# Kernel optimization log

Measured on AMD Instinct MI355X. Metric: run time of the kernel, lower is better.

## Reference

```python
import jax, jax.numpy as jnp
import numpy as np

B = 16384
HIST_LEN, DYN_DIM, STAT_DIM, TIME_DIM = 24, 8, 3, 8
N_STATIONS, EMB_DIM = 120, 16
IN_DIM = HIST_LEN * DYN_DIM + STAT_DIM + TIME_DIM + EMB_DIM  # 219
HIDDEN, OUT = 64, 1
GRID, K = 5, 3
NUM_BASIS = GRID + K  # 8


def make_grid(in_dim):
    # uniform extended grid on [-1, 1], pykan-style: G + 2k + 1 knots per input
    h = 2.0 / GRID
    pts = jnp.arange(-K, GRID + K + 1, dtype=jnp.float32) * h - 1.0  # [G+2k+1]
    return jnp.broadcast_to(pts, (in_dim, pts.shape[0]))


def b_splines(x, grid_pts):
    # x: [B, I], grid_pts: [I, G+2k+1] -> bases [B, I, G+k] via Cox-de Boor
    g = grid_pts[None]              # [1, I, M]
    xe = x[..., None]               # [B, I, 1]
    b = ((xe >= g[..., :-1]) & (xe < g[..., 1:])).astype(x.dtype)
    for p in range(1, K + 1):
        b = ((xe - g[..., : -(p + 1)]) / (g[..., p:-1] - g[..., : -(p + 1)]) * b[..., :-1]
             + (g[..., p + 1:] - xe) / (g[..., p + 1:] - g[..., 1:-p]) * b[..., 1:])
    return b  # [B, I, G+k]


def kan_layer(x, w_base, coef, grid_pts):
    # base path (silu residual) + spline path
    y_base = jax.nn.silu(x) @ w_base                              # [B, O]
    y_spline = jnp.einsum('big,iog->bo', b_splines(x, grid_pts), coef)
    return y_base + y_spline


def setup_inputs() -> dict:
    key = jax.random.key(0)
    ks = jax.random.split(key, 9)
    hist = jax.random.normal(ks[0], (B, HIST_LEN, DYN_DIM), dtype=jnp.float32)
    static = jax.random.normal(ks[1], (B, STAT_DIM), dtype=jnp.float32)
    time_feats = jax.random.normal(ks[2], (B, TIME_DIM), dtype=jnp.float32)
    st_idx = jax.random.randint(ks[3], (B,), 0, N_STATIONS)
    emb_table = jax.random.normal(ks[4], (N_STATIONS, EMB_DIM), dtype=jnp.float32)
    s1 = 1.0 / np.sqrt(IN_DIM)
    s2 = 1.0 / np.sqrt(HIDDEN)
    w_base1 = jax.random.normal(ks[5], (IN_DIM, HIDDEN), dtype=jnp.float32) * s1
    coef1 = jax.random.normal(ks[6], (IN_DIM, HIDDEN, NUM_BASIS), dtype=jnp.float32) * (0.1 * s1)
    w_base2 = jax.random.normal(ks[7], (HIDDEN, OUT), dtype=jnp.float32) * s2
    coef2 = jax.random.normal(ks[8], (HIDDEN, OUT, NUM_BASIS), dtype=jnp.float32) * (0.1 * s2)
    return {"hist": hist, "static": static, "time_feats": time_feats, "st_idx": st_idx,
            "emb_table": emb_table, "w_base1": w_base1, "coef1": coef1,
            "w_base2": w_base2, "coef2": coef2}


def reference(hist, static, time_feats, st_idx, emb_table, w_base1, coef1, w_base2, coef2):
    grid1 = make_grid(IN_DIM)
    grid2 = make_grid(HIDDEN)
    hist_flat = hist.reshape(hist.shape[0], -1)          # [B, hist_len*dyn_dim]
    emb = emb_table[st_idx]                              # [B, emb_dim]
    x = jnp.concatenate([hist_flat, static, time_feats, emb], axis=1)  # [B, 219]
    h = kan_layer(x, w_base1, coef1, grid1)              # [B, 64]
    out = kan_layer(h, w_base2, coef2, grid2)            # [B, 1]
    return out.squeeze(-1)                               # [B]
```

## Files before the change

### kernel.cpp

```cpp
#include <hip/hip_runtime.h>


typedef _Float16 half8 __attribute__((ext_vector_type(8)));
typedef float floatx4 __attribute__((ext_vector_type(4)));

#define NTILES 7
#define QSTEPS 9
#define FROW   296

__device__ __forceinline__ float silu_f(float x) {
    return x / (1.0f + __expf(-x));
}

__device__ __forceinline__ void bspline8(float x, float f[8]) {
    float u  = (x + 2.2f) * 2.5f;
    float fj = floorf(u);
    float t  = u - fj;
    int   j  = (int)fj;
    bool valid = (u >= 0.0f) && (u < 11.0f);
    float t2 = t * t, t3 = t2 * t;
    float omt = 1.0f - t;
    float b0 = omt * omt * omt * (1.0f / 6.0f);
    float b1 = (3.0f * t3 - 6.0f * t2 + 4.0f) * (1.0f / 6.0f);
    float b2 = (-3.0f * t3 + 3.0f * t2 + 3.0f * t + 1.0f) * (1.0f / 6.0f);
    float b3 = t3 * (1.0f / 6.0f);
    if (!valid) { b0 = b1 = b2 = b3 = 0.0f; }
    int base = j - 3;
#pragma unroll
    for (int g = 0; g < 8; ++g) {
        int m = g - base;
        float v = (m == 0) ? b0 : 0.0f;
        v = (m == 1) ? b1 : v;
        v = (m == 2) ? b2 : v;
        v = (m == 3) ? b3 : v;
        f[g] = v;
    }
}

__global__ __launch_bounds__(256) void build_w(
    const float* __restrict__ wb1, const float* __restrict__ cf1,
    _Float16* __restrict__ wcat)
{
    int flat = blockIdx.x * 256 + threadIdx.x;
    int j    = flat & 7;
    int l    = (flat >> 3) & 63;
    int nt   = (flat >> 9) & 3;
    int step = flat >> 11;
    int t    = step / QSTEPS;
    int q    = step - t * QSTEPS;
    int kl   = q * 32 + ((l >> 4) << 3) + j;
    int n    = nt * 16 + (l & 15);
    float v  = 0.0f;
    if (kl < 32) {
        int i = t * 32 + kl;
        if (i < 219) v = wb1[i * 64 + n];
    } else {
        int sp = kl - 32;
        int i  = t * 32 + (sp >> 3);
        int g  = sp & 7;
        if (i < 219) v = cf1[(i * 64 + n) * 8 + g];
    }
    wcat[flat] = (_Float16)v;
}

__global__ __launch_bounds__(256) void kan_mfma(
    const float* __restrict__ hist,
    const float* __restrict__ statf,
    const float* __restrict__ timef,
    const int*   __restrict__ st_idx,
    const float* __restrict__ emb,
    const _Float16* __restrict__ wcat,
    const float* __restrict__ wb2,
    const float* __restrict__ cf2,
    float* __restrict__ out)
{
    __shared__ union {
        _Float16 feat[32 * FROW];
        struct { float h[32 * 65]; float part[8 * 32]; } ep;
    } sm;

    const int tid  = threadIdx.x;
    const int lane = tid & 63;
    const int w    = __builtin_amdgcn_readfirstlane(tid >> 6);
    const int bx   = blockIdx.x;

    const int iloc = tid & 31;
    const int sg   = tid >> 5;

    floatx4 acc[2];
    acc[0] = (floatx4){0.f, 0.f, 0.f, 0.f};
    acc[1] = (floatx4){0.f, 0.f, 0.f, 0.f};

    for (int t = 0; t < NTILES; ++t) {
        const int i = t * 32 + iloc;
        __syncthreads();
#pragma unroll
        for (int r = 0; r < 4; ++r) {
            const int s = sg * 4 + r;
            const int b = bx * 32 + s;
            float sv = 0.0f;
            half8 spl = (half8)(_Float16)0.0f;
            if (i < 219) {
                float x;
                if (i < 192)      x = hist[b * 192 + i];
                else if (i < 195) x = statf[b * 3 + (i - 192)];
                else if (i < 203) x = timef[b * 8 + (i - 195)];
                else              x = emb[st_idx[b] * 16 + (i - 203)];
                sv = silu_f(x);
                float f[8];
                bspline8(x, f);
#pragma unroll
                for (int g = 0; g < 8; ++g) spl[g] = (_Float16)f[g];
            }
            sm.feat[s * FROW + iloc] = (_Float16)sv;
            *(half8*)&sm.feat[s * FROW + 32 + iloc * 8] = spl;
        }
        __syncthreads();
#pragma unroll
        for (int q = 0; q < QSTEPS; ++q) {
            half8 bfrag = *(const half8*)(wcat + (size_t)(((t * QSTEPS + q) * 4 + w) * 64 + lane) * 8);
            const int koff = q * 32 + ((lane >> 4) << 3);
#pragma unroll
            for (int mt = 0; mt < 2; ++mt) {
                half8 afrag = *(const half8*)&sm.feat[(mt * 16 + (lane & 15)) * FROW + koff];
                acc[mt] = __builtin_amdgcn_mfma_f32_16x16x32_f16(afrag, bfrag, acc[mt], 0, 0, 0);
            }
        }
    }

    __syncthreads();
#pragma unroll
    for (int mt = 0; mt < 2; ++mt) {
#pragma unroll
        for (int r = 0; r < 4; ++r) {
            const int row = mt * 16 + ((lane >> 4) << 2) + r;
            const int col = w * 16 + (lane & 15);
            sm.ep.h[row * 65 + col] = acc[mt][r];
        }
    }
    __syncthreads();

    {
        const int s  = tid & 31;
        const int og = tid >> 5;
        float psum = 0.0f;
#pragma unroll
        for (int oo = 0; oo < 8; ++oo) {
            const int o = og * 8 + oo;
            float h = sm.ep.h[s * 65 + o];
            psum = fmaf(silu_f(h), wb2[o], psum);
            float f2[8];
            bspline8(h, f2);
#pragma unroll
            for (int g = 0; g < 8; ++g)
                psum = fmaf(f2[g], cf2[o * 8 + g], psum);
        }
        sm.ep.part[og * 32 + s] = psum;
    }
    __syncthreads();
    if (tid < 32) {
        float r = 0.0f;
#pragma unroll
        for (int og = 0; og < 8; ++og) r += sm.ep.part[og * 32 + tid];
        out[bx * 32 + tid] = r;
    }
}

extern "C" void kernel_launch(void* const* d_in, const int* in_sizes, int n_in,
                              void* d_out, int out_size, void* d_ws, size_t ws_size,
                              hipStream_t stream) {
    const float* hist  = (const float*)d_in[0];
    const float* statf = (const float*)d_in[1];
    const float* timef = (const float*)d_in[2];
    const int*   stidx = (const int*)  d_in[3];
    const float* emb   = (const float*)d_in[4];
    const float* wb1   = (const float*)d_in[5];
    const float* cf1   = (const float*)d_in[6];
    const float* wb2   = (const float*)d_in[7];
    const float* cf2   = (const float*)d_in[8];
    float* out = (float*)d_out;

    _Float16* wcat = (_Float16*)d_ws;

    build_w<<<504, 256, 0, stream>>>(wb1, cf1, wcat);
    kan_mfma<<<512, 256, 0, stream>>>(hist, statf, timef, stidx, emb,
                                      wcat, wb2, cf2, out);
}
```

Before: 110.4 us.

## Stage raw inputs in LDS and build MFMA A-fragments in registers with split-K waves

The kernel now loads raw x values into shared memory once with vectorized float4 loads. Each wave computes its silu and B-spline A-fragments directly in registers: the spline fragment comes from a 64-bit shift of four packed fp16 basis values, replacing the dense 8-way select and the fp16 feature tile in LDS. The weight layout is reordered so that each K-step holds either 32 silu inputs or 4 inputs × 8 bases. Waves split M and K, and the two K halves are summed in the epilogue. This removes the per-tile barriers and the LDS feature writes, but each wave now recomputes the features for its own rows.

```diff
diff --git a/kernel.cpp b/kernel.cpp
--- a/kernel.cpp
+++ b/kernel.cpp
@@ -4,22 +4,19 @@
 typedef _Float16 half8 __attribute__((ext_vector_type(8)));
 typedef float floatx4 __attribute__((ext_vector_type(4)));
 
-#define NTILES 7
-#define QSTEPS 9
-#define FROW   296
+#define XR 233
 
 __device__ __forceinline__ float silu_f(float x) {
     return x / (1.0f + __expf(-x));
 }
 
-__device__ __forceinline__ void bspline8(float x, float f[8]) {
+__device__ __forceinline__ void bspline8_dense(float x, float f[8]) {
     float u  = (x + 2.2f) * 2.5f;
     float fj = floorf(u);
     float t  = u - fj;
     int   j  = (int)fj;
     bool valid = (u >= 0.0f) && (u < 11.0f);
-    float t2 = t * t, t3 = t2 * t;
-    float omt = 1.0f - t;
+    float t2 = t * t, t3 = t2 * t, omt = 1.0f - t;
     float b0 = omt * omt * omt * (1.0f / 6.0f);
     float b1 = (3.0f * t3 - 6.0f * t2 + 4.0f) * (1.0f / 6.0f);
     float b2 = (-3.0f * t3 + 3.0f * t2 + 3.0f * t + 1.0f) * (1.0f / 6.0f);
@@ -37,30 +34,62 @@
     }
 }
 
+__device__ __forceinline__ half8 bspline_frag(float x) {
+    float u  = (x + 2.2f) * 2.5f;
+    float fj = floorf(u);
+    float t  = u - fj;
+    int   j  = (int)fj;
+    bool valid = (u >= 0.0f) && (u < 11.0f);
+    float t2 = t * t, t3 = t2 * t, omt = 1.0f - t;
+    float b0 = omt * omt * omt * (1.0f / 6.0f);
+    float b1 = (3.0f * t3 - 6.0f * t2 + 4.0f) * (1.0f / 6.0f);
+    float b2 = (-3.0f * t3 + 3.0f * t2 + 3.0f * t + 1.0f) * (1.0f / 6.0f);
+    float b3 = t3 * (1.0f / 6.0f);
+    union { _Float16 h[4]; unsigned long long q; } p;
+    p.h[0] = (_Float16)b0; p.h[1] = (_Float16)b1;
+    p.h[2] = (_Float16)b2; p.h[3] = (_Float16)b3;
+    unsigned long long lo = valid ? p.q : 0ull;
+    int jc = valid ? j : 3;
+    int sh = (jc - 3) * 16;
+    unsigned long long rlo, rhi;
+    if (sh >= 0) {
+        rlo = (sh < 64) ? (lo << sh) : 0ull;
+        rhi = (sh == 0) ? 0ull
+            : (sh < 64) ? (lo >> (64 - sh))
+                        : (lo << (sh - 64));
+    } else {
+        rlo = lo >> (-sh);
+        rhi = 0ull;
+    }
+    union { unsigned long long q[2]; half8 v; } r;
+    r.q[0] = rlo; r.q[1] = rhi;
+    return r.v;
+}
+
 __global__ __launch_bounds__(256) void build_w(
     const float* __restrict__ wb1, const float* __restrict__ cf1,
     _Float16* __restrict__ wcat)
 {
     int flat = blockIdx.x * 256 + threadIdx.x;
-    int j    = flat & 7;
-    int l    = (flat >> 3) & 63;
-    int nt   = (flat >> 9) & 3;
-    int step = flat >> 11;
-    int t    = step / QSTEPS;
-    int q    = step - t * QSTEPS;
-    int kl   = q * 32 + ((l >> 4) << 3) + j;
-    int n    = nt * 16 + (l & 15);
-    float v  = 0.0f;
-    if (kl < 32) {
-        int i = t * 32 + kl;
-        if (i < 219) v = wb1[i * 64 + n];
+    int lane = flat & 63;
+    int nt   = (flat >> 6) & 3;
+    int st   = flat >> 8;
+    int kg   = lane >> 4;
+    int n    = nt * 16 + (lane & 15);
+    _Float16 v[8];
+    if (st < 7) {
+#pragma unroll
+        for (int j = 0; j < 8; ++j) {
+            int i = st * 32 + kg * 8 + j;
+            v[j] = (_Float16)((i < 219) ? wb1[i * 64 + n] : 0.0f);
+        }
     } else {
-        int sp = kl - 32;
-        int i  = t * 32 + (sp >> 3);
-        int g  = sp & 7;
-        if (i < 219) v = cf1[(i * 64 + n) * 8 + g];
-    }
-    wcat[flat] = (_Float16)v;
+        int i = (st - 7) * 4 + kg;
+#pragma unroll
+        for (int j = 0; j < 8; ++j)
+            v[j] = (_Float16)((i < 219) ? cf1[(i * 64 + n) * 8 + j] : 0.0f);
+    }
+    *(half8*)(wcat + (size_t)flat * 8) = *(half8*)v;
 }
 
 __global__ __launch_bounds__(256) void kan_mfma(
@@ -75,67 +104,95 @@
     float* __restrict__ out)
 {
     __shared__ union {
-        _Float16 feat[32 * FROW];
-        struct { float h[32 * 65]; float part[8 * 32]; } ep;
+        float xb[32 * XR];
+        struct { float h[2][32 * 65]; float part[8 * 32]; } ep;
     } sm;
 
     const int tid  = threadIdx.x;
     const int lane = tid & 63;
     const int w    = __builtin_amdgcn_readfirstlane(tid >> 6);
+    const int mt   = w & 1;
+    const int kh   = w >> 1;
     const int bx   = blockIdx.x;
-
-    const int iloc = tid & 31;
-    const int sg   = tid >> 5;
-
-    floatx4 acc[2];
-    acc[0] = (floatx4){0.f, 0.f, 0.f, 0.f};
-    acc[1] = (floatx4){0.f, 0.f, 0.f, 0.f};
-
-    for (int t = 0; t < NTILES; ++t) {
-        const int i = t * 32 + iloc;
-        __syncthreads();
+    const int row  = lane & 15;
+    const int kg   = lane >> 4;
+
+    {
+        const int s = tid >> 3, q4 = tid & 7;
+        const int b = bx * 32 + s;
+        const float4* h4 = (const float4*)hist;
+#pragma unroll
+        for (int f = 0; f < 6; ++f) {
+            int i4 = q4 + 8 * f;
+            float4 v = h4[b * 48 + i4];
+            sm.xb[s * XR + i4 * 4 + 0] = v.x;
+            sm.xb[s * XR + i4 * 4 + 1] = v.y;
+            sm.xb[s * XR + i4 * 4 + 2] = v.z;
+            sm.xb[s * XR + i4 * 4 + 3] = v.w;
+        }
+    }
+#pragma unroll
+    for (int f = 0; f < 4; ++f) {
+        int flat = f * 256 + tid;
+        int s  = flat >> 5;
+        int ii = 192 + (flat & 31);
+        int b  = bx * 32 + s;
+        float v;
+        if (ii < 195)      v = statf[b * 3 + (ii - 192)];
+        else if (ii < 203) v = timef[b * 8 + (ii - 195)];
+        else if (ii < 219) v = emb[st_idx[b] * 16 + (ii - 203)];
+        else               v = 0.0f;
+        sm.xb[s * XR + ii] = v;
+    }
+    __syncthreads();
+
+    const float* xrow = &sm.xb[(mt * 16 + row) * XR];
+
+    floatx4 acc[4];
+#pragma unroll
+    for (int nt = 0; nt < 4; ++nt) acc[nt] = (floatx4){0.f, 0.f, 0.f, 0.f};
+
+    for (int st = kh; st < 7; st += 2) {
+        const _Float16* wp = wcat + (size_t)(st * 4) * 512 + lane * 8;
+        half8 bf0 = *(const half8*)(wp);
+        half8 bf1 = *(const half8*)(wp + 512);
+        half8 bf2 = *(const half8*)(wp + 1024);
+        half8 bf3 = *(const half8*)(wp + 1536);
+        const int i0 = st * 32 + kg * 8;
+        half8 af;
+#pragma unroll
+        for (int jj = 0; jj < 8; ++jj)
+            af[jj] = (_Float16)silu_f(xrow[i0 + jj]);
+        acc[0] = __builtin_amdgcn_mfma_f32_16x16x32_f16(af, bf0, acc[0], 0, 0, 0);
+        acc[1] = __builtin_amdgcn_mfma_f32_16x16x32_f16(af, bf1, acc[1], 0, 0, 0);
+        acc[2] = __builtin_amdgcn_mfma_f32_16x16x32_f16(af, bf2, acc[2], 0, 0, 0);
+        acc[3] = __builtin_amdgcn_mfma_f32_16x16x32_f16(af, bf3, acc[3], 0, 0, 0);
+    }
+
+    const int st0 = (kh == 1) ? 7 : 8;
+#pragma unroll 2
+    for (int st = st0; st < 63; st += 2) {
+        const _Float16* wp = wcat + (size_t)(st * 4) * 512 + lane * 8;
+        half8 bf0 = *(const half8*)(wp);
+        half8 bf1 = *(const half8*)(wp + 512);
+        half8 bf2 = *(const half8*)(wp + 1024);
+        half8 bf3 = *(const half8*)(wp + 1536);
+        float x = xrow[(st - 7) * 4 + kg];
+        half8 af = bspline_frag(x);
+        acc[0] = __builtin_amdgcn_mfma_f32_16x16x32_f16(af, bf0, acc[0], 0, 0, 0);
+        acc[1] = __builtin_amdgcn_mfma_f32_16x16x32_f16(af, bf1, acc[1], 0, 0, 0);
+        acc[2] = __builtin_amdgcn_mfma_f32_16x16x32_f16(af, bf2, acc[2], 0, 0, 0);
+        acc[3] = __builtin_amdgcn_mfma_f32_16x16x32_f16(af, bf3, acc[3], 0, 0, 0);
+    }
+
+    __syncthreads();
+#pragma unroll
+    for (int nt = 0; nt < 4; ++nt) {
 #pragma unroll
         for (int r = 0; r < 4; ++r) {
-            const int s = sg * 4 + r;
-            const int b = bx * 32 + s;
-            float sv = 0.0f;
-            half8 spl = (half8)(_Float16)0.0f;
-            if (i < 219) {
-                float x;
-                if (i < 192)      x = hist[b * 192 + i];
-                else if (i < 195) x = statf[b * 3 + (i - 192)];
-                else if (i < 203) x = timef[b * 8 + (i - 195)];
-                else              x = emb[st_idx[b] * 16 + (i - 203)];
-                sv = silu_f(x);
-                float f[8];
-                bspline8(x, f);
-#pragma unroll
-                for (int g = 0; g < 8; ++g) spl[g] = (_Float16)f[g];
-            }
-            sm.feat[s * FROW + iloc] = (_Float16)sv;
-            *(half8*)&sm.feat[s * FROW + 32 + iloc * 8] = spl;
-        }
-        __syncthreads();
-#pragma unroll
-        for (int q = 0; q < QSTEPS; ++q) {
-            half8 bfrag = *(const half8*)(wcat + (size_t)(((t * QSTEPS + q) * 4 + w) * 64 + lane) * 8);
-            const int koff = q * 32 + ((lane >> 4) << 3);
-#pragma unroll
-            for (int mt = 0; mt < 2; ++mt) {
-                half8 afrag = *(const half8*)&sm.feat[(mt * 16 + (lane & 15)) * FROW + koff];
-                acc[mt] = __builtin_amdgcn_mfma_f32_16x16x32_f16(afrag, bfrag, acc[mt], 0, 0, 0);
-            }
-        }
-    }
-
-    __syncthreads();
-#pragma unroll
-    for (int mt = 0; mt < 2; ++mt) {
-#pragma unroll
-        for (int r = 0; r < 4; ++r) {
-            const int row = mt * 16 + ((lane >> 4) << 2) + r;
-            const int col = w * 16 + (lane & 15);
-            sm.ep.h[row * 65 + col] = acc[mt][r];
+            const int rr = mt * 16 + kg * 4 + r;
+            const int cc = nt * 16 + row;
+            sm.ep.h[kh][rr * 65 + cc] = acc[nt][r];
         }
     }
     __syncthreads();
@@ -147,10 +204,10 @@
 #pragma unroll
         for (int oo = 0; oo < 8; ++oo) {
             const int o = og * 8 + oo;
-            float h = sm.ep.h[s * 65 + o];
+            float h = sm.ep.h[0][s * 65 + o] + sm.ep.h[1][s * 65 + o];
             psum = fmaf(silu_f(h), wb2[o], psum);
             float f2[8];
-            bspline8(h, f2);
+            bspline8_dense(h, f2);
 #pragma unroll
             for (int g = 0; g < 8; ++g)
                 psum = fmaf(f2[g], cf2[o * 8 + g], psum);
@@ -182,7 +239,7 @@
 
     _Float16* wcat = (_Float16*)d_ws;
 
-    build_w<<<504, 256, 0, stream>>>(wb1, cf1, wcat);
+    build_w<<<63, 256, 0, stream>>>(wb1, cf1, wcat);
     kan_mfma<<<512, 256, 0, stream>>>(hist, statf, timef, stidx, emb,
                                       wcat, wb2, cf2, out);
 }
```

After: 94.08 us. -14.8%, faster.
